# Kernel optimization log

Hardware: AMD Instinct MI355X
Metric: run time of the kernel (lower is better)

The kernel has to match this reference:

```python
import jax, jax.numpy as jnp
import numpy as np

HIDDEN = 1024
NUM_HEADS = 16
HEAD_DIM = HIDDEN // NUM_HEADS


def setup_inputs() -> dict:
    key = jax.random.key(0)
    ks = jax.random.split(key, 5)
    scale = 1.0 / np.sqrt(HIDDEN)
    x = jax.random.normal(ks[0], (2, 2048, HIDDEN), dtype=jnp.float32)
    qkv_w = jax.random.uniform(ks[1], (3 * HIDDEN, HIDDEN), jnp.float32, -scale, scale)
    qkv_b = jax.random.uniform(ks[2], (3 * HIDDEN,), jnp.float32, -scale, scale)
    out_w = jax.random.uniform(ks[3], (HIDDEN, HIDDEN), jnp.float32, -scale, scale)
    out_b = jax.random.uniform(ks[4], (HIDDEN,), jnp.float32, -scale, scale)
    return {"x": x, "qkv_w": qkv_w, "qkv_b": qkv_b, "out_w": out_w, "out_b": out_b}


def reference(x, qkv_w, qkv_b, out_w, out_b):
    B, S, _ = x.shape
    qkv = jnp.einsum('bsd,ed->bse', x, qkv_w) + qkv_b  # [B,S,3H]
    q, k, v = jnp.split(qkv, 3, axis=-1)
    # [B,S,H] -> [B,nh,S,hd]
    def to_heads(t):
        return t.reshape(B, S, NUM_HEADS, HEAD_DIM).transpose(0, 2, 1, 3)
    q, k, v = to_heads(q), to_heads(k), to_heads(v)
    scores = jnp.einsum('bhqd,bhkd->bhqk', q, k) / np.sqrt(HEAD_DIM).astype(np.float32)
    attn = jax.nn.softmax(scores, axis=-1)
    o = jnp.einsum('bhqk,bhkd->bhqd', attn, v)
    o = o.transpose(0, 2, 1, 3).reshape(B, S, HIDDEN)
    return jnp.einsum('bsd,ed->bse', o, out_w) + out_b
```

## Files before the change

kernel.cpp:

```cpp
#include <hip/hip_runtime.h>
#include <stdint.h>

typedef __bf16 bf16x8 __attribute__((ext_vector_type(8)));
typedef float  f32x4  __attribute__((ext_vector_type(4)));
typedef float  f32x16 __attribute__((ext_vector_type(16)));
typedef unsigned short u16;
typedef unsigned int   u32;

#define B_  2
#define S_  2048
#define H_  1024
#define NH_ 16
#define HD_ 64
#define QSCL 0.18033688011112042f

__device__ __forceinline__ u16 f2bf(float f) {
  u32 u = __builtin_bit_cast(u32, f);
  return (u16)((u + 0x7FFFu + ((u >> 16) & 1u)) >> 16);
}
__device__ __forceinline__ float ex2(float x) { return __builtin_amdgcn_exp2f(x); }
__device__ __forceinline__ u32 cvtpk(float lo, float hi) {
  u32 r; asm("v_cvt_pk_bf16_f32 %0, %1, %2" : "=v"(r) : "v"(lo), "v"(hi)); return r;
}
__device__ __forceinline__ void gload_lds16(const u16* g, u16* lds) {
  __builtin_amdgcn_global_load_lds(
      (__attribute__((address_space(1))) void*)(void*)g,
      (__attribute__((address_space(3))) void*)lds, 16, 0, 0);
}
#define SBAR() asm volatile("s_barrier" ::: "memory")

__global__ void cvt_all(const float* __restrict__ a, const float* __restrict__ b,
                        const float* __restrict__ c, u16* __restrict__ oa,
                        u16* __restrict__ ob, u16* __restrict__ oc) {
  int i = blockIdx.x * 256 + threadIdx.x;
  const float4* src; ushort4* dst; int j;
  if (i < 1048576)      { src = (const float4*)a; dst = (ushort4*)oa; j = i; }
  else if (i < 1835008) { src = (const float4*)b; dst = (ushort4*)ob; j = i - 1048576; }
  else                  { src = (const float4*)c; dst = (ushort4*)oc; j = i - 1835008; }
  const float4 v = src[j];
  ushort4 o;
  o.x = f2bf(v.x); o.y = f2bf(v.y); o.z = f2bf(v.z); o.w = f2bf(v.w);
  dst[j] = o;
}

__global__ __launch_bounds__(256, 2)
void gemm_qkv(const u16* __restrict__ A, const u16* __restrict__ W,
              const float* __restrict__ bias,
              u16* __restrict__ qb, u16* __restrict__ kb, u16* __restrict__ vtb)
{
  __shared__ __align__(16) u16 smem[40960];
  u16* const Vt = smem;
  const int K = 1024;
  const int tid = threadIdx.x;
  const int w = tid >> 6, l = tid & 63;
  const int lg = l >> 4, lr = l & 15;
  const int wm = w >> 1, wn = w & 1;
  const int tM = blockIdx.y * 128, tN = blockIdx.x * 192;

  f32x4 acc[4][6] = {};

  const int srow = l >> 3;
  const int scol = ((l & 7) ^ srow) << 3;
  const u16* asrc = A + (size_t)(tM + w * 32 + srow) * K + scol;
  const u16* bsrc = W + (size_t)(tN + w * 48 + srow) * K + scol;

  auto STG = [&](int buf, int k0) {
#pragma unroll
    for (int j = 0; j < 4; ++j)
      gload_lds16(asrc + (size_t)(j * 8) * K + k0, &smem[buf * 8192 + (w * 32 + j * 8) * 64]);
#pragma unroll
    for (int j = 0; j < 6; ++j)
      gload_lds16(bsrc + (size_t)(j * 8) * K + k0, &smem[16384 + buf * 12288 + (w * 48 + j * 8) * 64]);
  };

  STG(0, 0);
  asm volatile("s_waitcnt vmcnt(0)" ::: "memory");
  SBAR();

  const int sw = lr & 7;

  for (int t = 0; t < 16; ++t) {
    const int cur = t & 1;
    if (t + 1 < 16) STG(cur ^ 1, (t + 1) * 64);

    bf16x8 af[4][2];
#pragma unroll
    for (int m = 0; m < 4; ++m)
#pragma unroll
      for (int kk = 0; kk < 2; ++kk)
        af[m][kk] = *(const bf16x8*)&smem[cur * 8192 + (wm * 64 + m * 16 + lr) * 64 +
                                          (((kk * 4 + lg) ^ sw) << 3)];
    __builtin_amdgcn_s_setprio(1);
#pragma unroll
    for (int n = 0; n < 6; ++n) {
      bf16x8 bw0 = *(const bf16x8*)&smem[16384 + cur * 12288 + (wn * 96 + n * 16 + lr) * 64 + (((lg) ^ sw) << 3)];
      bf16x8 bw1 = *(const bf16x8*)&smem[16384 + cur * 12288 + (wn * 96 + n * 16 + lr) * 64 + (((4 + lg) ^ sw) << 3)];
#pragma unroll
      for (int m = 0; m < 4; ++m) {
        acc[m][n] = __builtin_amdgcn_mfma_f32_16x16x32_bf16(af[m][0], bw0, acc[m][n], 0, 0, 0);
        acc[m][n] = __builtin_amdgcn_mfma_f32_16x16x32_bf16(af[m][1], bw1, acc[m][n], 0, 0, 0);
      }
    }
    __builtin_amdgcn_s_setprio(0);

    asm volatile("s_waitcnt vmcnt(0)" ::: "memory");
    SBAR();
  }

  const int bb = tM >> 11, ssb = tM & 2047;
#pragma unroll
  for (int n = 0; n < 6; ++n) {
    const int cl = wn * 96 + n * 16 + lr;
    const int col = tN + cl;
    const float bv = bias[col];
    const int t3 = col >> 10, rem = col & 1023;
    const int hh = rem >> 6, dd = rem & 63;
    if (t3 < 2) {
      const float sc = (t3 == 0) ? QSCL : 1.f;
      u16* dst = (t3 == 0) ? qb : kb;
#pragma unroll
      for (int m = 0; m < 4; ++m)
#pragma unroll
        for (int r = 0; r < 4; ++r) {
          const int row = tM + wm * 64 + m * 16 + lg * 4 + r;
          dst[((size_t)(bb * NH_ + hh) * S_ + (row & 2047)) * HD_ + dd] = f2bf((acc[m][n][r] + bv) * sc);
        }
    } else {
#pragma unroll
      for (int m = 0; m < 4; ++m) {
        ushort4 pk;
        pk.x = f2bf(acc[m][n][0] + bv);
        pk.y = f2bf(acc[m][n][1] + bv);
        pk.z = f2bf(acc[m][n][2] + bv);
        pk.w = f2bf(acc[m][n][3] + bv);
        *(ushort4*)&Vt[cl * 136 + wm * 64 + m * 16 + lg * 4] = pk;
      }
    }
  }

  if (tN >= 1920) {
    __syncthreads();
    const int cl0 = (tN < 2048) ? (2048 - tN) : 0;
    const int nch = (192 - cl0) * 16;
    for (int c = tid; c < nch; c += 256) {
      const int cv = cl0 + (c >> 4), ch = c & 15;
      const int rem = (tN + cv) & 1023;
      const int hh2 = rem >> 6, dd2 = rem & 63;
      const uint4 v = *(const uint4*)&Vt[cv * 136 + ch * 8];
      *(uint4*)&vtb[((size_t)(bb * NH_ + hh2) * HD_ + dd2) * S_ + ssb + ch * 8] = v;
    }
  }
}

__global__ __launch_bounds__(256, 2)
void gemm_out(const u16* __restrict__ A, const u16* __restrict__ W,
              const float* __restrict__ bias, float* __restrict__ outf)
{
  __shared__ __align__(16) u16 Al[2][128 * 64];
  __shared__ __align__(16) u16 Bl[2][64 * 64];
  const int K = 1024, N = 1024;
  const int tid = threadIdx.x;
  const int w = tid >> 6, l = tid & 63;
  const int lg = l >> 4, lr = l & 15;
  const int tM = blockIdx.y * 128, tN = blockIdx.x * 64;

  f32x4 acc[2][4] = {};

  const int srow = l >> 3;
  const int scol = ((l & 7) ^ srow) << 3;
  const u16* asrc = A + (size_t)(tM + w * 32 + srow) * K + scol;
  const u16* bsrc = W + (size_t)(tN + w * 16 + srow) * K + scol;

  auto STG = [&](int buf, int k0) {
#pragma unroll
    for (int j = 0; j < 4; ++j)
      gload_lds16(asrc + (size_t)(j * 8) * K + k0, &Al[buf][(w * 32 + j * 8) * 64]);
#pragma unroll
    for (int j = 0; j < 2; ++j)
      gload_lds16(bsrc + (size_t)(j * 8) * K + k0, &Bl[buf][(w * 16 + j * 8) * 64]);
  };

  STG(0, 0);
  asm volatile("s_waitcnt vmcnt(0)" ::: "memory");
  SBAR();

  const int sw = lr & 7;

  for (int t = 0; t < 16; ++t) {
    const int cur = t & 1;
    if (t + 1 < 16) STG(cur ^ 1, (t + 1) * 64);

    bf16x8 af[2][2];
#pragma unroll
    for (int m = 0; m < 2; ++m)
#pragma unroll
      for (int kk = 0; kk < 2; ++kk)
        af[m][kk] = *(const bf16x8*)&Al[cur][(w * 32 + m * 16 + lr) * 64 +
                                            (((kk * 4 + lg) ^ sw) << 3)];
    __builtin_amdgcn_s_setprio(1);
#pragma unroll
    for (int n = 0; n < 4; ++n) {
      bf16x8 bw0 = *(const bf16x8*)&Bl[cur][(n * 16 + lr) * 64 + (((lg) ^ sw) << 3)];
      bf16x8 bw1 = *(const bf16x8*)&Bl[cur][(n * 16 + lr) * 64 + (((4 + lg) ^ sw) << 3)];
#pragma unroll
      for (int m = 0; m < 2; ++m) {
        acc[m][n] = __builtin_amdgcn_mfma_f32_16x16x32_bf16(af[m][0], bw0, acc[m][n], 0, 0, 0);
        acc[m][n] = __builtin_amdgcn_mfma_f32_16x16x32_bf16(af[m][1], bw1, acc[m][n], 0, 0, 0);
      }
    }
    __builtin_amdgcn_s_setprio(0);

    asm volatile("s_waitcnt vmcnt(0)" ::: "memory");
    SBAR();
  }

#pragma unroll
  for (int n = 0; n < 4; ++n) {
    const int col = tN + n * 16 + lr;
    const float bv = bias[col];
#pragma unroll
    for (int m = 0; m < 2; ++m)
#pragma unroll
      for (int r = 0; r < 4; ++r) {
        const int row = tM + w * 32 + m * 16 + lg * 4 + r;
        outf[(size_t)row * N + col] = acc[m][n][r] + bv;
      }
  }
}

__global__ __launch_bounds__(256, 2)
void attn_fwd(const u16* __restrict__ qb, const u16* __restrict__ kb,
              const u16* __restrict__ vtb, u16* __restrict__ ob)
{
  __shared__ __align__(16) u16 Kl[2][2][64 * 64];
  __shared__ __align__(16) u16 Vl[2][2][64 * 64];

  const int tid = threadIdx.x;
  const int w = tid >> 6, l = tid & 63;
  const int q32 = l & 31, hi = l >> 5;
  const int idx = blockIdx.x;
  const int bh = idx & 31, qt = idx >> 5;
  const int bb = bh >> 4, hh = bh & 15;
  const int q0 = qt * 128 + w * 32;

  bf16x8 qf[4];
#pragma unroll
  for (int ks = 0; ks < 4; ++ks)
    qf[ks] = *(const bf16x8*)&qb[((size_t)bh * S_ + q0 + q32) * HD_ + ks * 16 + hi * 8];

  const f32x16 z16 = {};
  f32x16 acc[2] = {z16, z16};
  float lrun = 0.f;

  const int srow = l >> 3;
  const int scol = ((l & 7) ^ srow) << 3;
  const u16* kbase = kb  + ((size_t)bh * S_  + w * 16 + srow) * HD_ + scol;
  const u16* vbase = vtb + ((size_t)bh * HD_ + w * 16 + srow) * S_  + scol;

  auto STAGE = [&](int buf, int t) {
#pragma unroll
    for (int s = 0; s < 2; ++s)
#pragma unroll
      for (int j = 0; j < 2; ++j) {
        gload_lds16(kbase + ((size_t)t * 128 + s * 64) * HD_ + j * 8 * HD_,
                    &Kl[buf][s][(w * 16 + j * 8) * 64]);
        gload_lds16(vbase + (size_t)t * 128 + s * 64 + j * 8 * S_,
                    &Vl[buf][s][(w * 16 + j * 8) * 64]);
      }
  };

  STAGE(0, 0);
  __syncthreads();

  const int sw = q32 & 7;

  auto SOFTMAX = [&](f32x16& st0, f32x16& st1, bf16x8* pa) {
#pragma unroll
    for (int kt = 0; kt < 2; ++kt) {
      const f32x16& stt = kt ? st1 : st0;
      float p[16];
#pragma unroll
      for (int r = 0; r < 16; ++r) p[r] = ex2(stt[r]);
#pragma unroll
      for (int g = 0; g < 4; ++g)
        lrun += (p[4 * g] + p[4 * g + 1]) + (p[4 * g + 2] + p[4 * g + 3]);
      u32 wk0[4], wk1[4];
#pragma unroll
      for (int g = 0; g < 4; ++g) {
        wk0[g] = cvtpk(p[4 * g], p[4 * g + 1]);
        wk1[g] = cvtpk(p[4 * g + 2], p[4 * g + 3]);
      }
#pragma unroll
      for (int k2 = 0; k2 < 2; ++k2) {
        u32 a0 = wk0[2 * k2], b0 = wk0[2 * k2 + 1];
        u32 a1 = wk1[2 * k2], b1 = wk1[2 * k2 + 1];
        asm volatile("v_permlane32_swap_b32 %0, %1" : "+v"(a0), "+v"(b0));
        asm volatile("v_permlane32_swap_b32 %0, %1" : "+v"(a1), "+v"(b1));
        uint4 wv = {a0, a1, b0, b1};
        pa[kt * 2 + k2] = __builtin_bit_cast(bf16x8, wv);
      }
    }
  };

  for (int t = 0; t < 16; ++t) {
    const int cur = t & 1;
    if (t + 1 < 16) STAGE(cur ^ 1, t + 1);

    f32x16 stA0 = z16, stA1 = z16, stB0 = z16, stB1 = z16;
    __builtin_amdgcn_s_setprio(1);
#pragma unroll
    for (int ks = 0; ks < 4; ++ks) {
      const int so = ((((ks << 1) | hi) ^ sw) << 3);
      const bf16x8 kfA0 = *(const bf16x8*)&Kl[cur][0][(q32) * 64 + so];
      const bf16x8 kfA1 = *(const bf16x8*)&Kl[cur][0][(32 + q32) * 64 + so];
      const bf16x8 kfB0 = *(const bf16x8*)&Kl[cur][1][(q32) * 64 + so];
      const bf16x8 kfB1 = *(const bf16x8*)&Kl[cur][1][(32 + q32) * 64 + so];
      stA0 = __builtin_amdgcn_mfma_f32_32x32x16_bf16(kfA0, qf[ks], stA0, 0, 0, 0);
      stA1 = __builtin_amdgcn_mfma_f32_32x32x16_bf16(kfA1, qf[ks], stA1, 0, 0, 0);
      stB0 = __builtin_amdgcn_mfma_f32_32x32x16_bf16(kfB0, qf[ks], stB0, 0, 0, 0);
      stB1 = __builtin_amdgcn_mfma_f32_32x32x16_bf16(kfB1, qf[ks], stB1, 0, 0, 0);
    }
    __builtin_amdgcn_s_setprio(0);

    bf16x8 pa[4];
    SOFTMAX(stA0, stA1, pa);
    __builtin_amdgcn_s_setprio(1);
#pragma unroll
    for (int dt = 0; dt < 2; ++dt)
#pragma unroll
      for (int ks = 0; ks < 4; ++ks) {
        const bf16x8 vf = *(const bf16x8*)&Vl[cur][0][(dt * 32 + q32) * 64 + ((((ks << 1) | hi) ^ sw) << 3)];
        acc[dt] = __builtin_amdgcn_mfma_f32_32x32x16_bf16(vf, pa[ks], acc[dt], 0, 0, 0);
      }
    __builtin_amdgcn_s_setprio(0);

    SOFTMAX(stB0, stB1, pa);
    __builtin_amdgcn_s_setprio(1);
#pragma unroll
    for (int dt = 0; dt < 2; ++dt)
#pragma unroll
      for (int ks = 0; ks < 4; ++ks) {
        const bf16x8 vf = *(const bf16x8*)&Vl[cur][1][(dt * 32 + q32) * 64 + ((((ks << 1) | hi) ^ sw) << 3)];
        acc[dt] = __builtin_amdgcn_mfma_f32_32x32x16_bf16(vf, pa[ks], acc[dt], 0, 0, 0);
      }
    __builtin_amdgcn_s_setprio(0);

    __syncthreads();
  }

  lrun += __shfl_xor(lrun, 32);
  const float linv = 1.f / lrun;
  const size_t orow = ((size_t)(bb * S_ + q0 + q32)) * H_ + hh * HD_;
#pragma unroll
  for (int dt = 0; dt < 2; ++dt)
#pragma unroll
    for (int g = 0; g < 4; ++g) {
      const u32 o0 = cvtpk(acc[dt][4 * g] * linv, acc[dt][4 * g + 1] * linv);
      const u32 o1 = cvtpk(acc[dt][4 * g + 2] * linv, acc[dt][4 * g + 3] * linv);
      uint2 ov; ov.x = o0; ov.y = o1;
      *(uint2*)&ob[orow + dt * 32 + g * 8 + hi * 4] = ov;
    }
}

extern "C" void kernel_launch(void* const* d_in, const int* in_sizes, int n_in,
                              void* d_out, int out_size, void* d_ws, size_t ws_size,
                              hipStream_t stream) {
  const float* x     = (const float*)d_in[0];
  const float* qkv_w = (const float*)d_in[1];
  const float* qkv_b = (const float*)d_in[2];
  const float* out_w = (const float*)d_in[3];
  const float* out_b = (const float*)d_in[4];

  char* ws = (char*)d_ws;
  u16* xb    = (u16*)(ws);
  u16* wqkvb = (u16*)(ws + 8388608);
  u16* wob   = (u16*)(ws + 14680064);
  u16* qb    = (u16*)(ws + 16777216);
  u16* kb    = (u16*)(ws + 25165824);
  u16* vtb   = (u16*)(ws + 33554432);
  u16* ob    = (u16*)(ws + 41943040);

  cvt_all<<<8192, 256, 0, stream>>>(x, qkv_w, out_w, xb, wqkvb, wob);

  gemm_qkv<<<dim3(16, 32), 256, 0, stream>>>(xb, wqkvb, qkv_b, qb, kb, vtb);
  attn_fwd<<<512, 256, 0, stream>>>(qb, kb, vtb, ob);
  gemm_out<<<dim3(16, 32), 256, 0, stream>>>(ob, wob, out_b, (float*)d_out);
}
```

Baseline: 98.12 us.

## Use 8 waves and triple-buffered LDS prefetch in QKV GEMM

The QKV projection GEMM moves from 4 waves to 8 waves per block, each wave now owning half as many N columns. The LDS staging goes from double to triple buffering with a two-tile-ahead prefetch and partial vmcnt waits, so global loads overlap more compute. In exchange, LDS use per block grows to 120 KB and occupancy drops to one block per CU, and each wave holds a smaller accumulator tile.

```diff
diff --git a/kernel.cpp b/kernel.cpp
--- a/kernel.cpp
+++ b/kernel.cpp
@@ -43,58 +43,63 @@
   dst[j] = o;
 }
 
-__global__ __launch_bounds__(256, 2)
+__global__ __launch_bounds__(512, 1)
 void gemm_qkv(const u16* __restrict__ A, const u16* __restrict__ W,
               const float* __restrict__ bias,
               u16* __restrict__ qb, u16* __restrict__ kb, u16* __restrict__ vtb)
 {
-  __shared__ __align__(16) u16 smem[40960];
+  __shared__ __align__(16) u16 smem[61440];
   u16* const Vt = smem;
   const int K = 1024;
   const int tid = threadIdx.x;
   const int w = tid >> 6, l = tid & 63;
   const int lg = l >> 4, lr = l & 15;
-  const int wm = w >> 1, wn = w & 1;
+  const int wm = w >> 2, wn = w & 3;
   const int tM = blockIdx.y * 128, tN = blockIdx.x * 192;
 
-  f32x4 acc[4][6] = {};
-
-  const int srow = l >> 3;
-  const int scol = ((l & 7) ^ srow) << 3;
-  const u16* asrc = A + (size_t)(tM + w * 32 + srow) * K + scol;
-  const u16* bsrc = W + (size_t)(tN + w * 48 + srow) * K + scol;
+  f32x4 acc[4][3] = {};
+
+  const int srow = tid >> 3;
+  const int scol = ((tid & 7) ^ (srow & 7)) << 3;
+  const u16* asrc = A + (size_t)(tM + srow) * K + scol;
+  const u16* bsrc = W + (size_t)(tN + srow) * K + scol;
 
   auto STG = [&](int buf, int k0) {
 #pragma unroll
-    for (int j = 0; j < 4; ++j)
-      gload_lds16(asrc + (size_t)(j * 8) * K + k0, &smem[buf * 8192 + (w * 32 + j * 8) * 64]);
-#pragma unroll
-    for (int j = 0; j < 6; ++j)
-      gload_lds16(bsrc + (size_t)(j * 8) * K + k0, &smem[16384 + buf * 12288 + (w * 48 + j * 8) * 64]);
+    for (int p = 0; p < 2; ++p)
+      gload_lds16(asrc + (size_t)(p * 64) * K + k0, &smem[buf * 8192 + p * 4096 + w * 512]);
+#pragma unroll
+    for (int p = 0; p < 3; ++p)
+      gload_lds16(bsrc + (size_t)(p * 64) * K + k0, &smem[24576 + buf * 12288 + p * 4096 + w * 512]);
   };
 
   STG(0, 0);
-  asm volatile("s_waitcnt vmcnt(0)" ::: "memory");
+  STG(1, 64);
+  asm volatile("s_waitcnt vmcnt(5)" ::: "memory");
   SBAR();
 
   const int sw = lr & 7;
 
+  int cur = 0;
   for (int t = 0; t < 16; ++t) {
-    const int cur = t & 1;
-    if (t + 1 < 16) STG(cur ^ 1, (t + 1) * 64);
+    if (t + 2 < 16) {
+      int nb = cur + 2; if (nb >= 3) nb -= 3;
+      STG(nb, (t + 2) * 64);
+    }
+    const int aoff = cur * 8192, boff = 24576 + cur * 12288;
 
     bf16x8 af[4][2];
 #pragma unroll
     for (int m = 0; m < 4; ++m)
 #pragma unroll
       for (int kk = 0; kk < 2; ++kk)
-        af[m][kk] = *(const bf16x8*)&smem[cur * 8192 + (wm * 64 + m * 16 + lr) * 64 +
+        af[m][kk] = *(const bf16x8*)&smem[aoff + (wm * 64 + m * 16 + lr) * 64 +
                                           (((kk * 4 + lg) ^ sw) << 3)];
     __builtin_amdgcn_s_setprio(1);
 #pragma unroll
-    for (int n = 0; n < 6; ++n) {
-      bf16x8 bw0 = *(const bf16x8*)&smem[16384 + cur * 12288 + (wn * 96 + n * 16 + lr) * 64 + (((lg) ^ sw) << 3)];
-      bf16x8 bw1 = *(const bf16x8*)&smem[16384 + cur * 12288 + (wn * 96 + n * 16 + lr) * 64 + (((4 + lg) ^ sw) << 3)];
+    for (int n = 0; n < 3; ++n) {
+      bf16x8 bw0 = *(const bf16x8*)&smem[boff + (wn * 48 + n * 16 + lr) * 64 + (((lg) ^ sw) << 3)];
+      bf16x8 bw1 = *(const bf16x8*)&smem[boff + (wn * 48 + n * 16 + lr) * 64 + (((4 + lg) ^ sw) << 3)];
 #pragma unroll
       for (int m = 0; m < 4; ++m) {
         acc[m][n] = __builtin_amdgcn_mfma_f32_16x16x32_bf16(af[m][0], bw0, acc[m][n], 0, 0, 0);
@@ -103,14 +108,16 @@
     }
     __builtin_amdgcn_s_setprio(0);
 
-    asm volatile("s_waitcnt vmcnt(0)" ::: "memory");
+    if (t + 2 < 16)      asm volatile("s_waitcnt vmcnt(5)" ::: "memory");
+    else if (t + 1 < 16) asm volatile("s_waitcnt vmcnt(0)" ::: "memory");
     SBAR();
+    cur = (cur + 1 == 3) ? 0 : cur + 1;
   }
 
   const int bb = tM >> 11, ssb = tM & 2047;
 #pragma unroll
-  for (int n = 0; n < 6; ++n) {
-    const int cl = wn * 96 + n * 16 + lr;
+  for (int n = 0; n < 3; ++n) {
+    const int cl = wn * 48 + n * 16 + lr;
     const int col = tN + cl;
     const float bv = bias[col];
     const int t3 = col >> 10, rem = col & 1023;
@@ -122,8 +129,8 @@
       for (int m = 0; m < 4; ++m)
 #pragma unroll
         for (int r = 0; r < 4; ++r) {
-          const int row = tM + wm * 64 + m * 16 + lg * 4 + r;
-          dst[((size_t)(bb * NH_ + hh) * S_ + (row & 2047)) * HD_ + dd] = f2bf((acc[m][n][r] + bv) * sc);
+          const int rl = wm * 64 + m * 16 + lg * 4 + r;
+          dst[((size_t)(bb * NH_ + hh) * S_ + (ssb + rl)) * HD_ + dd] = f2bf((acc[m][n][r] + bv) * sc);
         }
     } else {
 #pragma unroll
@@ -142,7 +149,7 @@
     __syncthreads();
     const int cl0 = (tN < 2048) ? (2048 - tN) : 0;
     const int nch = (192 - cl0) * 16;
-    for (int c = tid; c < nch; c += 256) {
+    for (int c = tid; c < nch; c += 512) {
       const int cv = cl0 + (c >> 4), ch = c & 15;
       const int rem = (tN + cv) & 1023;
       const int hh2 = rem >> 6, dd2 = rem & 63;
@@ -382,7 +389,7 @@
 
   cvt_all<<<8192, 256, 0, stream>>>(x, qkv_w, out_w, xb, wqkvb, wob);
 
-  gemm_qkv<<<dim3(16, 32), 256, 0, stream>>>(xb, wqkvb, qkv_b, qb, kb, vtb);
+  gemm_qkv<<<dim3(16, 32), 512, 0, stream>>>(xb, wqkvb, qkv_b, qb, kb, vtb);
   attn_fwd<<<512, 256, 0, stream>>>(qb, kb, vtb, ob);
   gemm_out<<<dim3(16, 32), 256, 0, stream>>>(ob, wob, out_b, (float*)d_out);
 }
```

Result: slower. 101.0 us (+2.9%).
